# Performance work log

Hardware: AMD Instinct MI355X
Metric: run time of the kernel (lower is better)

The kernel has to match this reference:

```python
import jax, jax.numpy as jnp
import numpy as np

DIMENSIONS = 10000
NUM_LEVELS = 256
SIZE = 28
BATCH = 64
NUM_CLASSES = 10


def _bipolar(key, shape):
    # torchhd MAP hypervectors are random +/-1
    return jnp.where(jax.random.uniform(key, shape) > 0.5, 1.0, -1.0).astype(jnp.float32)


def setup_inputs() -> dict:
    key = jax.random.key(0)
    kx, kpx, kpy, kv, kw = jax.random.split(key, 5)
    # pixel intensities in [0, 1]
    x = jax.random.uniform(kx, (BATCH, SIZE, SIZE), dtype=jnp.float32)
    # position = hard_quantize(bundle(px, py)) with px, py random bipolar HVs
    px = _bipolar(kpx, (SIZE * SIZE, DIMENSIONS))
    py = _bipolar(kpy, (SIZE * SIZE, DIMENSIONS))
    position = jnp.where(px + py > 0, 1.0, -1.0).astype(jnp.float32)
    # Level embedding table (bipolar hypervectors per intensity level)
    level_weight = _bipolar(kv, (NUM_LEVELS, DIMENSIONS))
    # classify Linear weight (zero in original; small random here so output is non-trivial)
    classify_weight = jax.random.normal(kw, (NUM_CLASSES, DIMENSIONS), jnp.float32) * 0.01
    return {"x": x, "position": position, "level_weight": level_weight,
            "classify_weight": classify_weight}


def reference(x, position, level_weight, classify_weight):
    B = x.shape[0]
    xf = x.reshape(B, -1)                                   # [B, P] with P = size*size
    # torchhd Level: value in [0,1] -> round to one of NUM_LEVELS indices
    idx = jnp.clip(jnp.round(xf * (NUM_LEVELS - 1)), 0, NUM_LEVELS - 1).astype(jnp.int32)
    # bind: gather level HVs and elementwise-multiply with position HVs, then multiset-bundle (sum over P)
    bundled = jnp.einsum('bpd,pd->bd', level_weight[idx], position)  # [B, D]
    # hard_quantize: sign threshold (>0 -> 1, else -1)
    enc = jnp.where(bundled > 0, 1.0, -1.0).astype(x.dtype)
    # classify: Linear(DIMENSIONS, num_classes, bias=False)
    logit = enc @ classify_weight.T                          # [B, num_classes]
    return logit
```

## Files before the change

### kernel.cpp

```cpp
#include <hip/hip_runtime.h>
#include <stdint.h>

#define D      10000
#define WPR    313
#define NPIX   784
#define NB     64
#define NC     10
#define NPC    16
#define PCL    49

__global__ __launch_bounds__(320) void pack_kernel(const float* __restrict__ lev,
                                                   const float* __restrict__ pos,
                                                   uint32_t* __restrict__ Lp,
                                                   uint32_t* __restrict__ Pp,
                                                   float* __restrict__ out) {
    if (blockIdx.x == 0)
        for (int i = threadIdx.x; i < NB * NC; i += 320) out[i] = 0.0f;

    int row = blockIdx.x;
    const float* src; uint32_t* dst;
    if (row < 256) { src = lev + (size_t)row * D;        dst = Lp + row * WPR; }
    else           { src = pos + (size_t)(row - 256) * D; dst = Pp + (row - 256) * WPR; }

    int w = threadIdx.x;
    if (w >= WPR) return;
    const uint4* p4 = (const uint4*)((const uint32_t*)src + w * 32);
    uint32_t word = 0;
    if (w < WPR - 1) {
        #pragma unroll
        for (int k = 0; k < 8; ++k) {
            uint4 u = p4[k];
            word |= (u.x >> 31) << (4 * k)     | (u.y >> 31) << (4 * k + 1)
                  | (u.z >> 31) << (4 * k + 2) | (u.w >> 31) << (4 * k + 3);
        }
    } else {
        #pragma unroll
        for (int k = 0; k < 4; ++k) {
            uint4 u = p4[k];
            word |= (u.x >> 31) << (4 * k)     | (u.y >> 31) << (4 * k + 1)
                  | (u.z >> 31) << (4 * k + 2) | (u.w >> 31) << (4 * k + 3);
        }
    }
    dst[w] = word;
}

__global__ __launch_bounds__(64) void count_kernel(const float* __restrict__ x,
                                                   const uint32_t* __restrict__ Lp,
                                                   const uint32_t* __restrict__ Pp,
                                                   uint32_t* __restrict__ partial) {
    int tid = threadIdx.x;
    int b = blockIdx.y, pc = blockIdx.z;
    int w = blockIdx.x * 64 + tid;
    int p0 = pc * PCL;

    __shared__ int idxs[PCL];
    if (tid < PCL) {
        float xv = x[b * NPIX + p0 + tid];
        int v = (int)rintf(xv * 255.0f);
        v = v < 0 ? 0 : (v > 255 ? 255 : v);
        idxs[tid] = v * WPR;
    }
    __syncthreads();
    if (w >= WPR) return;

    uint32_t s0 = 0, s1 = 0, s2 = 0, s3 = 0, s4 = 0, s5 = 0;
    const uint32_t* pp = Pp + p0 * WPR + w;
    #pragma unroll 7
    for (int i = 0; i < PCL; ++i) {
        int ro = __builtin_amdgcn_readfirstlane(idxs[i]);
        uint32_t c = Lp[ro + w] ^ pp[(size_t)i * WPR];
        uint32_t t;
        t = s0 & c; s0 ^= c; c = t;
        t = s1 & c; s1 ^= c; c = t;
        t = s2 & c; s2 ^= c; c = t;
        t = s3 & c; s3 ^= c; c = t;
        t = s4 & c; s4 ^= c; c = t;
        s5 ^= c;
    }

    uint32_t* o = partial + (((size_t)pc * NB + b) * 8) * WPR + w;
    #pragma unroll
    for (int q = 0; q < 8; ++q) {
        uint32_t word = 0;
        #pragma unroll
        for (int r = 0; r < 4; ++r) {
            int j = q * 4 + r;
            uint32_t cnt = ((s0 >> j) & 1u)        | (((s1 >> j) & 1u) << 1)
                         | (((s2 >> j) & 1u) << 2) | (((s3 >> j) & 1u) << 3)
                         | (((s4 >> j) & 1u) << 4) | (((s5 >> j) & 1u) << 5);
            word |= cnt << (8 * r);
        }
        o[(size_t)q * WPR] = word;
    }
}

__global__ __launch_bounds__(256) void logits_kernel(const uint32_t* __restrict__ partial,
                                                     const float* __restrict__ cw,
                                                     float* __restrict__ out) {
    int b = blockIdx.y;
    int tid = threadIdx.x;
    int dend = blockIdx.x * 1280 + 1280; if (dend > D) dend = D;
    float acc[NC];
    #pragma unroll
    for (int c = 0; c < NC; ++c) acc[c] = 0.0f;

    for (int d = blockIdx.x * 1280 + tid; d < dend; d += 256) {
        int w = d >> 5, j = d & 31, q = j >> 2, shift = 8 * (j & 3);
        int sum = 0;
        #pragma unroll
        for (int pc = 0; pc < NPC; ++pc)
            sum += (int)((partial[(((size_t)pc * NB + b) * 8 + q) * WPR + w] >> shift) & 0xffu);
        float enc = (2 * sum < NPIX) ? 1.0f : -1.0f;
        #pragma unroll
        for (int c = 0; c < NC; ++c) acc[c] = fmaf(enc, cw[c * D + d], acc[c]);
    }

    int lane = tid & 63, wv = tid >> 6;
    __shared__ float red[4][NC];
    #pragma unroll
    for (int c = 0; c < NC; ++c) {
        float v = acc[c];
        #pragma unroll
        for (int off = 32; off > 0; off >>= 1) v += __shfl_down(v, off, 64);
        if (lane == 0) red[wv][c] = v;
    }
    __syncthreads();
    if (tid < NC) {
        float s = red[0][tid] + red[1][tid] + red[2][tid] + red[3][tid];
        atomicAdd(&out[b * NC + tid], s);
    }
}

extern "C" void kernel_launch(void* const* d_in, const int* in_sizes, int n_in,
                              void* d_out, int out_size, void* d_ws, size_t ws_size,
                              hipStream_t stream) {
    const float* x   = (const float*)d_in[0];
    const float* pos = (const float*)d_in[1];
    const float* lev = (const float*)d_in[2];
    const float* cw  = (const float*)d_in[3];
    float* out = (float*)d_out;

    uint32_t* Lp      = (uint32_t*)d_ws;
    uint32_t* Pp      = Lp + 256 * WPR;
    uint32_t* partial = Pp + NPIX * WPR;

    pack_kernel<<<256 + NPIX, 320, 0, stream>>>(lev, pos, Lp, Pp, out);
    dim3 g1(5, NB, NPC);
    count_kernel<<<g1, 64, 0, stream>>>(x, Lp, Pp, partial);
    dim3 g2(8, NB);
    logits_kernel<<<g2, 256, 0, stream>>>(partial, cw, out);
}
```

Measured before the change: 112.3 us.

## Fuse pack, count and logits into one cooperative kernel with grid syncs

Merges the three kernels into one persistent cooperative kernel that uses grid.sync between the bit-packing, popcount-accumulation and logits phases. It also changes the partial-count layout so each thread writes eight words as two 16-byte stores, and reads counts per word, summing bytes two lanes at a time. The sign multiply becomes an XOR of the float sign bit on vectorized classifier-weight loads. This removes two launch gaps and gives more coalesced memory traffic, at the cost of grid-wide barriers and a fixed grid of 512 blocks that does less parallel work in the count phase. A non-cooperative three-kernel fallback is kept.

```diff
diff --git a/kernel.cpp b/kernel.cpp
--- a/kernel.cpp
+++ b/kernel.cpp
@@ -1,5 +1,8 @@
 #include <hip/hip_runtime.h>
+#include <hip/hip_cooperative_groups.h>
 #include <stdint.h>
+
+namespace cg = cooperative_groups;
 
 #define D      10000
 #define WPR    313
@@ -8,67 +11,42 @@
 #define NC     10
 #define NPC    16
 #define PCL    49
-
-__global__ __launch_bounds__(320) void pack_kernel(const float* __restrict__ lev,
-                                                   const float* __restrict__ pos,
-                                                   uint32_t* __restrict__ Lp,
-                                                   uint32_t* __restrict__ Pp,
-                                                   float* __restrict__ out) {
-    if (blockIdx.x == 0)
-        for (int i = threadIdx.x; i < NB * NC; i += 320) out[i] = 0.0f;
-
-    int row = blockIdx.x;
+#define NROWS  (256 + NPIX)
+#define GRID   512
+#define BLK    256
+#define NT2    (NB * NPC * 5)
+
+__device__ __forceinline__ void pack_task(int task, const float* __restrict__ lev,
+                                          const float* __restrict__ pos,
+                                          uint32_t* __restrict__ Lp,
+                                          uint32_t* __restrict__ Pp) {
+    int row = task / WPR;
+    int w   = task - row * WPR;
     const float* src; uint32_t* dst;
-    if (row < 256) { src = lev + (size_t)row * D;        dst = Lp + row * WPR; }
+    if (row < 256) { src = lev + (size_t)row * D;         dst = Lp + row * WPR; }
     else           { src = pos + (size_t)(row - 256) * D; dst = Pp + (row - 256) * WPR; }
-
-    int w = threadIdx.x;
+    const uint4* p4 = (const uint4*)(src + w * 32);
+    uint32_t word = 0;
+    int kmax = (w < WPR - 1) ? 8 : 4;
+    for (int k = 0; k < kmax; ++k) {
+        uint4 u = p4[k];
+        word |= (u.x >> 31) << (4*k)     | (u.y >> 31) << (4*k + 1)
+              | (u.z >> 31) << (4*k + 2) | (u.w >> 31) << (4*k + 3);
+    }
+    dst[w] = word;
+}
+
+__device__ __forceinline__ void count_task(int b, int pc, int w, int vidx,
+                                           const uint32_t* __restrict__ Lp,
+                                           const uint32_t* __restrict__ Pp,
+                                           uint32_t* __restrict__ partial) {
     if (w >= WPR) return;
-    const uint4* p4 = (const uint4*)((const uint32_t*)src + w * 32);
-    uint32_t word = 0;
-    if (w < WPR - 1) {
-        #pragma unroll
-        for (int k = 0; k < 8; ++k) {
-            uint4 u = p4[k];
-            word |= (u.x >> 31) << (4 * k)     | (u.y >> 31) << (4 * k + 1)
-                  | (u.z >> 31) << (4 * k + 2) | (u.w >> 31) << (4 * k + 3);
-        }
-    } else {
-        #pragma unroll
-        for (int k = 0; k < 4; ++k) {
-            uint4 u = p4[k];
-            word |= (u.x >> 31) << (4 * k)     | (u.y >> 31) << (4 * k + 1)
-                  | (u.z >> 31) << (4 * k + 2) | (u.w >> 31) << (4 * k + 3);
-        }
-    }
-    dst[w] = word;
-}
-
-__global__ __launch_bounds__(64) void count_kernel(const float* __restrict__ x,
-                                                   const uint32_t* __restrict__ Lp,
-                                                   const uint32_t* __restrict__ Pp,
-                                                   uint32_t* __restrict__ partial) {
-    int tid = threadIdx.x;
-    int b = blockIdx.y, pc = blockIdx.z;
-    int w = blockIdx.x * 64 + tid;
-    int p0 = pc * PCL;
-
-    __shared__ int idxs[PCL];
-    if (tid < PCL) {
-        float xv = x[b * NPIX + p0 + tid];
-        int v = (int)rintf(xv * 255.0f);
-        v = v < 0 ? 0 : (v > 255 ? 255 : v);
-        idxs[tid] = v * WPR;
-    }
-    __syncthreads();
-    if (w >= WPR) return;
-
     uint32_t s0 = 0, s1 = 0, s2 = 0, s3 = 0, s4 = 0, s5 = 0;
-    const uint32_t* pp = Pp + p0 * WPR + w;
-    #pragma unroll 7
+    const uint32_t* pp = Pp + (pc * PCL) * WPR + w;
+    #pragma unroll
     for (int i = 0; i < PCL; ++i) {
-        int ro = __builtin_amdgcn_readfirstlane(idxs[i]);
-        uint32_t c = Lp[ro + w] ^ pp[(size_t)i * WPR];
+        int ro = __builtin_amdgcn_readlane(vidx, i);
+        uint32_t c = Lp[ro + w] ^ pp[i * WPR];
         uint32_t t;
         t = s0 & c; s0 ^= c; c = t;
         t = s1 & c; s1 ^= c; c = t;
@@ -77,8 +55,7 @@
         t = s4 & c; s4 ^= c; c = t;
         s5 ^= c;
     }
-
-    uint32_t* o = partial + (((size_t)pc * NB + b) * 8) * WPR + w;
+    uint32_t qw[8];
     #pragma unroll
     for (int q = 0; q < 8; ++q) {
         uint32_t word = 0;
@@ -90,33 +67,49 @@
                          | (((s4 >> j) & 1u) << 4) | (((s5 >> j) & 1u) << 5);
             word |= cnt << (8 * r);
         }
-        o[(size_t)q * WPR] = word;
-    }
-}
-
-__global__ __launch_bounds__(256) void logits_kernel(const uint32_t* __restrict__ partial,
-                                                     const float* __restrict__ cw,
-                                                     float* __restrict__ out) {
-    int b = blockIdx.y;
-    int tid = threadIdx.x;
-    int dend = blockIdx.x * 1280 + 1280; if (dend > D) dend = D;
+        qw[q] = word;
+    }
+    uint4* o = (uint4*)(partial + (((size_t)pc * NB + b) * WPR + w) * 8);
+    o[0] = make_uint4(qw[0], qw[1], qw[2], qw[3]);
+    o[1] = make_uint4(qw[4], qw[5], qw[6], qw[7]);
+}
+
+__device__ __forceinline__ void logits_task(int b, int ws, int tid,
+                                            const uint32_t* __restrict__ partial,
+                                            const float* __restrict__ cw,
+                                            float* __restrict__ out,
+                                            float (*red)[NC]) {
     float acc[NC];
     #pragma unroll
     for (int c = 0; c < NC; ++c) acc[c] = 0.0f;
 
-    for (int d = blockIdx.x * 1280 + tid; d < dend; d += 256) {
-        int w = d >> 5, j = d & 31, q = j >> 2, shift = 8 * (j & 3);
-        int sum = 0;
-        #pragma unroll
-        for (int pc = 0; pc < NPC; ++pc)
-            sum += (int)((partial[(((size_t)pc * NB + b) * 8 + q) * WPR + w] >> shift) & 0xffu);
-        float enc = (2 * sum < NPIX) ? 1.0f : -1.0f;
-        #pragma unroll
-        for (int c = 0; c < NC; ++c) acc[c] = fmaf(enc, cw[c * D + d], acc[c]);
-    }
-
+    for (int t = tid; t < 40 * 8; t += BLK) {
+        int wl = t >> 3, q = t & 7;
+        int w  = ws * 40 + wl;
+        int dbase = w * 32 + q * 4;
+        if (w < WPR && dbase < D) {
+            uint32_t aL = 0, aH = 0;
+            #pragma unroll
+            for (int pc = 0; pc < NPC; ++pc) {
+                uint32_t v = partial[(((size_t)pc * NB + b) * WPR + w) * 8 + q];
+                aL += v & 0x00FF00FFu;
+                aH += (v >> 8) & 0x00FF00FFu;
+            }
+            uint32_t c0 = aL & 0xFFFFu, c2 = aL >> 16;
+            uint32_t c1 = aH & 0xFFFFu, c3 = aH >> 16;
+            uint32_t g0 = (c0 >= 392u) ? 0x80000000u : 0u;
+            uint32_t g1 = (c1 >= 392u) ? 0x80000000u : 0u;
+            uint32_t g2 = (c2 >= 392u) ? 0x80000000u : 0u;
+            uint32_t g3 = (c3 >= 392u) ? 0x80000000u : 0u;
+            #pragma unroll
+            for (int c = 0; c < NC; ++c) {
+                uint4 cv = *(const uint4*)(cw + (size_t)c * D + dbase);
+                acc[c] += __uint_as_float(cv.x ^ g0) + __uint_as_float(cv.y ^ g1)
+                        + __uint_as_float(cv.z ^ g2) + __uint_as_float(cv.w ^ g3);
+            }
+        }
+    }
     int lane = tid & 63, wv = tid >> 6;
-    __shared__ float red[4][NC];
     #pragma unroll
     for (int c = 0; c < NC; ++c) {
         float v = acc[c];
@@ -125,10 +118,83 @@
         if (lane == 0) red[wv][c] = v;
     }
     __syncthreads();
-    if (tid < NC) {
-        float s = red[0][tid] + red[1][tid] + red[2][tid] + red[3][tid];
-        atomicAdd(&out[b * NC + tid], s);
-    }
+    if (tid < NC)
+        atomicAdd(&out[b * NC + tid],
+                  red[0][tid] + red[1][tid] + red[2][tid] + red[3][tid]);
+}
+
+__global__ __launch_bounds__(BLK, 2) void fused_kernel(
+    const float* __restrict__ x, const float* __restrict__ pos,
+    const float* __restrict__ lev, const float* __restrict__ cw,
+    uint32_t* __restrict__ Lp, uint32_t* __restrict__ Pp,
+    uint32_t* __restrict__ partial, float* __restrict__ out)
+{
+    cg::grid_group grid = cg::this_grid();
+    const int tid = threadIdx.x;
+    __shared__ float red[4][NC];
+
+    for (int task = blockIdx.x * BLK + tid; task < NROWS * WPR; task += GRID * BLK)
+        pack_task(task, lev, pos, Lp, Pp);
+    if (blockIdx.x == 0)
+        for (int i = tid; i < NB * NC; i += BLK) out[i] = 0.0f;
+    grid.sync();
+
+    {
+        int wid  = blockIdx.x * 4 + (tid >> 6);
+        int lane = tid & 63;
+        for (int t = wid; t < NT2; t += GRID * 4) {
+            int wb = t % 5;
+            int bt = t / 5;
+            int b  = bt & 63;
+            int pc = bt >> 6;
+            int vidx = 0;
+            if (lane < PCL) {
+                float xv = x[b * NPIX + pc * PCL + lane];
+                int v = (int)rintf(xv * 255.0f);
+                v = v < 0 ? 0 : (v > 255 ? 255 : v);
+                vidx = v * WPR;
+            }
+            count_task(b, pc, wb * 64 + lane, vidx, Lp, Pp, partial);
+        }
+    }
+    grid.sync();
+
+    logits_task(blockIdx.x >> 3, blockIdx.x & 7, tid, partial, cw, out, red);
+}
+
+__global__ __launch_bounds__(BLK) void pack_fb(const float* __restrict__ lev,
+                                               const float* __restrict__ pos,
+                                               uint32_t* __restrict__ Lp,
+                                               uint32_t* __restrict__ Pp,
+                                               float* __restrict__ out) {
+    for (int task = blockIdx.x * BLK + threadIdx.x; task < NROWS * WPR;
+         task += GRID * BLK)
+        pack_task(task, lev, pos, Lp, Pp);
+    if (blockIdx.x == 0)
+        for (int i = threadIdx.x; i < NB * NC; i += BLK) out[i] = 0.0f;
+}
+
+__global__ __launch_bounds__(64) void count_fb(const float* __restrict__ x,
+                                               const uint32_t* __restrict__ Lp,
+                                               const uint32_t* __restrict__ Pp,
+                                               uint32_t* __restrict__ partial) {
+    int lane = threadIdx.x;
+    int b = blockIdx.y, pc = blockIdx.z;
+    int vidx = 0;
+    if (lane < PCL) {
+        float xv = x[b * NPIX + pc * PCL + lane];
+        int v = (int)rintf(xv * 255.0f);
+        v = v < 0 ? 0 : (v > 255 ? 255 : v);
+        vidx = v * WPR;
+    }
+    count_task(b, pc, blockIdx.x * 64 + lane, vidx, Lp, Pp, partial);
+}
+
+__global__ __launch_bounds__(BLK) void logits_fb(const uint32_t* __restrict__ partial,
+                                                 const float* __restrict__ cw,
+                                                 float* __restrict__ out) {
+    __shared__ float red[4][NC];
+    logits_task(blockIdx.x >> 3, blockIdx.x & 7, threadIdx.x, partial, cw, out, red);
 }
 
 extern "C" void kernel_launch(void* const* d_in, const int* in_sizes, int n_in,
@@ -144,9 +210,13 @@
     uint32_t* Pp      = Lp + 256 * WPR;
     uint32_t* partial = Pp + NPIX * WPR;
 
-    pack_kernel<<<256 + NPIX, 320, 0, stream>>>(lev, pos, Lp, Pp, out);
-    dim3 g1(5, NB, NPC);
-    count_kernel<<<g1, 64, 0, stream>>>(x, Lp, Pp, partial);
-    dim3 g2(8, NB);
-    logits_kernel<<<g2, 256, 0, stream>>>(partial, cw, out);
-}
+    void* args[] = {(void*)&x, (void*)&pos, (void*)&lev, (void*)&cw,
+                    (void*)&Lp, (void*)&Pp, (void*)&partial, (void*)&out};
+    hipError_t err = hipLaunchCooperativeKernel((void*)fused_kernel, dim3(GRID),
+                                                dim3(BLK), args, 0, stream);
+    if (err != hipSuccess) {
+        pack_fb<<<GRID, BLK, 0, stream>>>(lev, pos, Lp, Pp, out);
+        count_fb<<<dim3(5, NB, NPC), 64, 0, stream>>>(x, Lp, Pp, partial);
+        logits_fb<<<GRID, BLK, 0, stream>>>(partial, cw, out);
+    }
+}
```

After: 252.7 us. 125% more time.

## Fuse bit-sliced counting with logits and flatten pack grid

Applied to the files above, without the earlier changes.

Merges the count and logits kernels into one fused kernel. Each block covers 64 words for one batch row, with 8 waves each counting 98 pixels into 7-bit bit-sliced counters. Per-wave byte counts are reduced in shared memory and thresholded, and the classifier weights are applied by sign-flipping through XOR on the float sign bit. This removes the global partial-count buffer and one kernel launch. The pack kernel now uses a flat thread-per-word grid instead of one block per row, but the fused kernel launches only 320 blocks.

```diff
diff --git a/kernel.cpp b/kernel.cpp
--- a/kernel.cpp
+++ b/kernel.cpp
@@ -6,79 +6,78 @@
 #define NPIX   784
 #define NB     64
 #define NC     10
-#define NPC    16
-#define PCL    49
+#define NROWS  (256 + NPIX)
+#define PCL    98
+#define BLK2   512
 
-__global__ __launch_bounds__(320) void pack_kernel(const float* __restrict__ lev,
+__global__ __launch_bounds__(256) void pack_kernel(const float* __restrict__ lev,
                                                    const float* __restrict__ pos,
                                                    uint32_t* __restrict__ Lp,
                                                    uint32_t* __restrict__ Pp,
                                                    float* __restrict__ out) {
     if (blockIdx.x == 0)
-        for (int i = threadIdx.x; i < NB * NC; i += 320) out[i] = 0.0f;
+        for (int i = threadIdx.x; i < NB * NC; i += 256) out[i] = 0.0f;
 
-    int row = blockIdx.x;
+    int task = blockIdx.x * 256 + threadIdx.x;
+    if (task >= NROWS * WPR) return;
+    int row = task / WPR;
+    int w   = task - row * WPR;
     const float* src; uint32_t* dst;
-    if (row < 256) { src = lev + (size_t)row * D;        dst = Lp + row * WPR; }
+    if (row < 256) { src = lev + (size_t)row * D;         dst = Lp + row * WPR; }
     else           { src = pos + (size_t)(row - 256) * D; dst = Pp + (row - 256) * WPR; }
-
-    int w = threadIdx.x;
-    if (w >= WPR) return;
-    const uint4* p4 = (const uint4*)((const uint32_t*)src + w * 32);
+    const uint4* p4 = (const uint4*)(src + w * 32);
     uint32_t word = 0;
-    if (w < WPR - 1) {
-        #pragma unroll
-        for (int k = 0; k < 8; ++k) {
-            uint4 u = p4[k];
-            word |= (u.x >> 31) << (4 * k)     | (u.y >> 31) << (4 * k + 1)
-                  | (u.z >> 31) << (4 * k + 2) | (u.w >> 31) << (4 * k + 3);
-        }
-    } else {
-        #pragma unroll
-        for (int k = 0; k < 4; ++k) {
-            uint4 u = p4[k];
-            word |= (u.x >> 31) << (4 * k)     | (u.y >> 31) << (4 * k + 1)
-                  | (u.z >> 31) << (4 * k + 2) | (u.w >> 31) << (4 * k + 3);
-        }
+    int kmax = (w < WPR - 1) ? 8 : 4;
+    for (int k = 0; k < kmax; ++k) {
+        uint4 u = p4[k];
+        word |= (u.x >> 31) << (4*k)     | (u.y >> 31) << (4*k + 1)
+              | (u.z >> 31) << (4*k + 2) | (u.w >> 31) << (4*k + 3);
     }
     dst[w] = word;
 }
 
-__global__ __launch_bounds__(64) void count_kernel(const float* __restrict__ x,
-                                                   const uint32_t* __restrict__ Lp,
-                                                   const uint32_t* __restrict__ Pp,
-                                                   uint32_t* __restrict__ partial) {
-    int tid = threadIdx.x;
-    int b = blockIdx.y, pc = blockIdx.z;
-    int w = blockIdx.x * 64 + tid;
-    int p0 = pc * PCL;
+__global__ __launch_bounds__(BLK2, 2) void fused_kernel(const float* __restrict__ x,
+                                                        const uint32_t* __restrict__ Lp,
+                                                        const uint32_t* __restrict__ Pp,
+                                                        const float* __restrict__ cw,
+                                                        float* __restrict__ out) {
+    const int tid  = threadIdx.x;
+    const int lane = tid & 63;
+    const int wv   = tid >> 6;
+    const int wg   = blockIdx.x;
+    const int b    = blockIdx.y;
 
-    __shared__ int idxs[PCL];
-    if (tid < PCL) {
-        float xv = x[b * NPIX + p0 + tid];
+    __shared__ int      idxs[NPIX];
+    __shared__ uint32_t qbuf[8][64][9];
+    __shared__ float    red[8][NC];
+
+    for (int i = tid; i < NPIX; i += BLK2) {
+        float xv = x[b * NPIX + i];
         int v = (int)rintf(xv * 255.0f);
         v = v < 0 ? 0 : (v > 255 ? 255 : v);
-        idxs[tid] = v * WPR;
+        idxs[i] = v * WPR;
     }
     __syncthreads();
-    if (w >= WPR) return;
 
-    uint32_t s0 = 0, s1 = 0, s2 = 0, s3 = 0, s4 = 0, s5 = 0;
-    const uint32_t* pp = Pp + p0 * WPR + w;
-    #pragma unroll 7
-    for (int i = 0; i < PCL; ++i) {
-        int ro = __builtin_amdgcn_readfirstlane(idxs[i]);
-        uint32_t c = Lp[ro + w] ^ pp[(size_t)i * WPR];
-        uint32_t t;
-        t = s0 & c; s0 ^= c; c = t;
-        t = s1 & c; s1 ^= c; c = t;
-        t = s2 & c; s2 ^= c; c = t;
-        t = s3 & c; s3 ^= c; c = t;
-        t = s4 & c; s4 ^= c; c = t;
-        s5 ^= c;
+    int w = wg * 64 + lane;
+    int p0 = wv * PCL;
+    uint32_t s0 = 0, s1 = 0, s2 = 0, s3 = 0, s4 = 0, s5 = 0, s6 = 0;
+    if (w < WPR) {
+        const uint32_t* pp = Pp + (size_t)p0 * WPR + w;
+        #pragma unroll 7
+        for (int i = 0; i < PCL; ++i) {
+            int ro = __builtin_amdgcn_readfirstlane(idxs[p0 + i]);
+            uint32_t c = Lp[ro + w] ^ pp[(size_t)i * WPR];
+            uint32_t t;
+            t = s0 & c; s0 ^= c; c = t;
+            t = s1 & c; s1 ^= c; c = t;
+            t = s2 & c; s2 ^= c; c = t;
+            t = s3 & c; s3 ^= c; c = t;
+            t = s4 & c; s4 ^= c; c = t;
+            t = s5 & c; s5 ^= c; c = t;
+            s6 ^= c;
+        }
     }
-
-    uint32_t* o = partial + (((size_t)pc * NB + b) * 8) * WPR + w;
     #pragma unroll
     for (int q = 0; q < 8; ++q) {
         uint32_t word = 0;
@@ -87,36 +86,43 @@
             int j = q * 4 + r;
             uint32_t cnt = ((s0 >> j) & 1u)        | (((s1 >> j) & 1u) << 1)
                          | (((s2 >> j) & 1u) << 2) | (((s3 >> j) & 1u) << 3)
-                         | (((s4 >> j) & 1u) << 4) | (((s5 >> j) & 1u) << 5);
+                         | (((s4 >> j) & 1u) << 4) | (((s5 >> j) & 1u) << 5)
+                         | (((s6 >> j) & 1u) << 6);
             word |= cnt << (8 * r);
         }
-        o[(size_t)q * WPR] = word;
+        qbuf[wv][lane][q] = word;
     }
-}
+    __syncthreads();
 
-__global__ __launch_bounds__(256) void logits_kernel(const uint32_t* __restrict__ partial,
-                                                     const float* __restrict__ cw,
-                                                     float* __restrict__ out) {
-    int b = blockIdx.y;
-    int tid = threadIdx.x;
-    int dend = blockIdx.x * 1280 + 1280; if (dend > D) dend = D;
     float acc[NC];
     #pragma unroll
     for (int c = 0; c < NC; ++c) acc[c] = 0.0f;
-
-    for (int d = blockIdx.x * 1280 + tid; d < dend; d += 256) {
-        int w = d >> 5, j = d & 31, q = j >> 2, shift = 8 * (j & 3);
-        int sum = 0;
-        #pragma unroll
-        for (int pc = 0; pc < NPC; ++pc)
-            sum += (int)((partial[(((size_t)pc * NB + b) * 8 + q) * WPR + w] >> shift) & 0xffu);
-        float enc = (2 * sum < NPIX) ? 1.0f : -1.0f;
-        #pragma unroll
-        for (int c = 0; c < NC; ++c) acc[c] = fmaf(enc, cw[c * D + d], acc[c]);
+    {
+        int wl = tid >> 3, q = tid & 7;
+        int w2 = wg * 64 + wl;
+        int dbase = w2 * 32 + q * 4;
+        if (w2 < WPR && dbase < D) {
+            uint32_t aL = 0, aH = 0;
+            #pragma unroll
+            for (int v = 0; v < 8; ++v) {
+                uint32_t u = qbuf[v][wl][q];
+                aL += u & 0x00FF00FFu;
+                aH += (u >> 8) & 0x00FF00FFu;
+            }
+            uint32_t c0 = aL & 0xFFFFu, c2 = aL >> 16;
+            uint32_t c1 = aH & 0xFFFFu, c3 = aH >> 16;
+            uint32_t g0 = (c0 >= 392u) ? 0x80000000u : 0u;
+            uint32_t g1 = (c1 >= 392u) ? 0x80000000u : 0u;
+            uint32_t g2 = (c2 >= 392u) ? 0x80000000u : 0u;
+            uint32_t g3 = (c3 >= 392u) ? 0x80000000u : 0u;
+            #pragma unroll
+            for (int c = 0; c < NC; ++c) {
+                uint4 cv = *(const uint4*)(cw + (size_t)c * D + dbase);
+                acc[c] += __uint_as_float(cv.x ^ g0) + __uint_as_float(cv.y ^ g1)
+                        + __uint_as_float(cv.z ^ g2) + __uint_as_float(cv.w ^ g3);
+            }
+        }
     }
-
-    int lane = tid & 63, wv = tid >> 6;
-    __shared__ float red[4][NC];
     #pragma unroll
     for (int c = 0; c < NC; ++c) {
         float v = acc[c];
@@ -126,7 +132,9 @@
     }
     __syncthreads();
     if (tid < NC) {
-        float s = red[0][tid] + red[1][tid] + red[2][tid] + red[3][tid];
+        float s = 0.0f;
+        #pragma unroll
+        for (int v = 0; v < 8; ++v) s += red[v][tid];
         atomicAdd(&out[b * NC + tid], s);
     }
 }
@@ -140,13 +148,9 @@
     const float* cw  = (const float*)d_in[3];
     float* out = (float*)d_out;
 
-    uint32_t* Lp      = (uint32_t*)d_ws;
-    uint32_t* Pp      = Lp + 256 * WPR;
-    uint32_t* partial = Pp + NPIX * WPR;
+    uint32_t* Lp = (uint32_t*)d_ws;
+    uint32_t* Pp = Lp + 256 * WPR;
 
-    pack_kernel<<<256 + NPIX, 320, 0, stream>>>(lev, pos, Lp, Pp, out);
-    dim3 g1(5, NB, NPC);
-    count_kernel<<<g1, 64, 0, stream>>>(x, Lp, Pp, partial);
-    dim3 g2(8, NB);
-    logits_kernel<<<g2, 256, 0, stream>>>(partial, cw, out);
+    pack_kernel<<<(NROWS * WPR + 255) / 256, 256, 0, stream>>>(lev, pos, Lp, Pp, out);
+    fused_kernel<<<dim3(5, NB), BLK2, 0, stream>>>(x, Lp, Pp, cw, out);
 }
```

Result: no change. 113.5 us (+1.1%).
